# Optimization experiments

Hardware: AMD Instinct MI355X
Metric: run time of the kernel (lower is better)

## Reference

```python
import jax, jax.numpy as jnp
import numpy as np

# Static graph/model dims
G, NPG, N = 64, 200, 12800          # graphs, nodes/graph, total nodes
EPG, E = 1000, 64000                # edges/graph, total edges
D, H, C = 1024, 3, 1024             # feature_size, heads, out channels/head
K1, K2, K3 = 160, 80, 16            # topk sizes: ceil(.8*200), .5*160, .2*80
NEG = -1e9


def _gat(x, src, dst, mask, W, att_s, att_d, b):
    """PyG GATConv (concat heads, add_self_loops=True, leaky_relu 0.2)."""
    n = x.shape[0]
    xw = (x @ W).reshape(n, H, C)                 # [n,H,C]
    a_s = (xw * att_s).sum(-1)                    # [n,H]
    a_d = (xw * att_d).sum(-1)
    loop = jnp.arange(n, dtype=src.dtype)
    s = jnp.concatenate([src, loop])
    d = jnp.concatenate([dst, loop])
    m = jnp.concatenate([mask, jnp.ones((n,), bool)])
    logit = jax.nn.leaky_relu(a_s[s] + a_d[d], 0.2)   # [E+n,H]
    logit = jnp.where(m[:, None], logit, NEG)
    mx = jax.ops.segment_max(logit, d, num_segments=n)
    ex = jnp.where(m[:, None], jnp.exp(logit - mx[d]), 0.0)
    den = jax.ops.segment_sum(ex, d, num_segments=n)
    alpha = ex / (den[d] + 1e-16)                 # segment softmax over dst
    out = jax.ops.segment_sum(alpha[:, :, None] * xw[s], d, num_segments=n)
    return out.reshape(n, H * C) + b


def _topk(x, src, dst, mask, p, n_in, k):
    """PyG TopKPooling: score=tanh(x.p/||p||), keep top-k per graph,
    scale kept rows by score; edge filtering realized as a mask."""
    score = jnp.tanh((x @ p) / jnp.linalg.norm(p))
    vals, idx = jax.lax.top_k(score.reshape(G, n_in), k)     # [G,k]
    perm = (idx + jnp.arange(G)[:, None] * n_in).reshape(-1)
    new_x = x[perm] * vals.reshape(-1, 1)
    newid = jnp.full((G * n_in,), -1, jnp.int32).at[perm].set(
        jnp.arange(G * k, dtype=jnp.int32))
    ns, nd = newid[src], newid[dst]
    nm = mask & (ns >= 0) & (nd >= 0)
    return new_x, jnp.where(nm, ns, 0), jnp.where(nm, nd, 0), nm


def _readout(x, k):
    xg = x.reshape(G, k, C)                       # contiguous equal graphs
    return jnp.concatenate([xg.max(1), xg.mean(1)], axis=1)  # [G,2C]


def setup_inputs() -> dict:
    key = jax.random.key(0)
    ks = jax.random.split(key, 32)
    x = jax.random.normal(ks[0], (N, D), jnp.float32)
    gid = jnp.repeat(jnp.arange(G, dtype=jnp.int32), EPG)
    src = jax.random.randint(ks[1], (E,), 0, NPG, jnp.int32) + gid * NPG
    dst = jax.random.randint(ks[2], (E,), 0, NPG, jnp.int32) + gid * NPG
    edge_index = jnp.stack([src, dst])
    batch_index = jnp.repeat(jnp.arange(G, dtype=jnp.int32), NPG)
    edge_attr = jnp.zeros((E, 1), jnp.float32)

    def gl(k, shape, fan):
        return jax.random.normal(k, shape, jnp.float32) * (1.0 / np.sqrt(fan))

    inp = dict(x=x, edge_attr=edge_attr, edge_index=edge_index,
               batch_index=batch_index)
    i = 3
    for L, fin in ((1, D), (2, C), (3, C)):
        inp[f'W{L}'] = gl(ks[i], (fin, H * C), fin); i += 1
        inp[f'as{L}'] = gl(ks[i], (H, C), C); i += 1
        inp[f'ad{L}'] = gl(ks[i], (H, C), C); i += 1
        inp[f'b{L}'] = jnp.zeros((H * C,), jnp.float32)
        inp[f'Wt{L}'] = gl(ks[i], (H * C, C), H * C); i += 1
        inp[f'bt{L}'] = jnp.zeros((C,), jnp.float32)
        inp[f'p{L}'] = gl(ks[i], (C,), C); i += 1
    inp['Wl1'] = gl(ks[i], (2 * C, 1024), 2 * C); i += 1
    inp['bl1'] = jnp.zeros((1024,), jnp.float32)
    inp['Wl2'] = gl(ks[i], (1024, 2), 1024); i += 1
    inp['bl2'] = jnp.zeros((2,), jnp.float32)
    return inp


def reference(x, edge_attr, edge_index, batch_index,
              W1, as1, ad1, b1, Wt1, bt1, p1,
              W2, as2, ad2, b2, Wt2, bt2, p2,
              W3, as3, ad3, b3, Wt3, bt3, p3,
              Wl1, bl1, Wl2, bl2):
    src, dst = edge_index[0], edge_index[1]
    mask = jnp.ones((src.shape[0],), bool)
    h = _gat(x, src, dst, mask, W1, as1, ad1, b1) @ Wt1 + bt1
    h, src, dst, mask = _topk(h, src, dst, mask, p1, NPG, K1)
    r1 = _readout(h, K1)
    h = _gat(h, src, dst, mask, W2, as2, ad2, b2) @ Wt2 + bt2
    h, src, dst, mask = _topk(h, src, dst, mask, p2, K1, K2)
    r2 = _readout(h, K2)
    h = _gat(h, src, dst, mask, W3, as3, ad3, b3) @ Wt3 + bt3
    h, src, dst, mask = _topk(h, src, dst, mask, p3, K2, K3)
    r3 = _readout(h, K3)
    z = r1 + r2 + r3                               # [G, 2C]
    z = jax.nn.relu(z @ Wl1 + bl1)                 # dropout inactive (eval)
    return z @ Wl2 + bl2                           # [G, 2]
```

## Files before the change

### kernel.cpp

```cpp
#include <hip/hip_runtime.h>
#include <math.h>

#define NG 64
#define EE 64000
#define HC3 3072
#define CC 1024

static inline int cdiv(int a, int b) { return (a + b - 1) / b; }

typedef float f4_t __attribute__((ext_vector_type(4)));
typedef short s8_t __attribute__((ext_vector_type(8)));

__device__ __forceinline__ float lrelu(float x) { return x > 0.f ? x : 0.2f * x; }
__device__ __forceinline__ unsigned fenc(float f) {
    unsigned u = __float_as_uint(f);
    return (u & 0x80000000u) ? ~u : (u | 0x80000000u);
}
__device__ __forceinline__ float fdec(unsigned e) {
    return (e & 0x80000000u) ? __uint_as_float(e ^ 0x80000000u) : __uint_as_float(~e);
}
__device__ __forceinline__ unsigned short f2bf(float f) {
    unsigned u = __float_as_uint(f);
    u += 0x7fffu + ((u >> 16) & 1u);
    return (unsigned short)(u >> 16);
}
__device__ __forceinline__ float bf2f(unsigned short h) {
    return __uint_as_float(((unsigned)h) << 16);
}
__device__ __forceinline__ void gll16(const unsigned short* g, unsigned short* l) {
    __builtin_amdgcn_global_load_lds(
        (const __attribute__((address_space(1))) void*)g,
        (__attribute__((address_space(3))) void*)l, 16, 0, 0);
}

__global__ __launch_bounds__(256) void gemm_split(
    const unsigned short* __restrict__ Ahi, const unsigned short* __restrict__ Alo, int lda,
    const unsigned short* __restrict__ Bhi, const unsigned short* __restrict__ Blo, int ldb,
    float* __restrict__ C, int ldc, int K,
    size_t zsA, size_t zsB, size_t zsC)
{
    __shared__ unsigned short sAH[128 * 32];
    __shared__ unsigned short sAL[128 * 32];
    __shared__ unsigned short sBH[128 * 32];
    __shared__ unsigned short sBL[128 * 32];

    Ahi += blockIdx.z * zsA; Alo += blockIdx.z * zsA;
    Bhi += blockIdx.z * zsB; Blo += blockIdx.z * zsB;
    C   += blockIdx.z * zsC;

    const int t = threadIdx.x;
    const int w = t >> 6, lane = t & 63;
    const int wr = w >> 1, wc = w & 1;
    const int row0 = blockIdx.y * 128, col0 = blockIdx.x * 128;

    const int srow = w * 16 + (lane >> 2);
    const int skg = (((lane & 3) ^ ((lane >> 3) & 3)) << 3);
    const size_t aoff0 = (size_t)(row0 + srow) * lda + skg;
    const size_t aoff1 = (size_t)(row0 + 64 + srow) * lda + skg;
    const size_t boff0 = (size_t)(col0 + srow) * ldb + skg;
    const size_t boff1 = (size_t)(col0 + 64 + srow) * ldb + skg;
    const int l0 = (w * 16) * 32;
    const int l1 = (64 + w * 16) * 32;

    f4_t acc[4][4];
    const f4_t z4 = {0.f, 0.f, 0.f, 0.f};
#pragma unroll
    for (int i = 0; i < 4; ++i)
#pragma unroll
        for (int j = 0; j < 4; ++j) acc[i][j] = z4;

    const int mrow0 = wr * 64 + (lane & 15);
    const int nrow0 = wc * 64 + (lane & 15);
    const int kslot = (((lane >> 4) ^ ((lane >> 1) & 3)) << 3);

    for (int k0 = 0; k0 < K; k0 += 32) {
        gll16(Ahi + aoff0 + k0, &sAH[l0]);
        gll16(Ahi + aoff1 + k0, &sAH[l1]);
        gll16(Alo + aoff0 + k0, &sAL[l0]);
        gll16(Alo + aoff1 + k0, &sAL[l1]);
        gll16(Bhi + boff0 + k0, &sBH[l0]);
        gll16(Bhi + boff1 + k0, &sBH[l1]);
        gll16(Blo + boff0 + k0, &sBL[l0]);
        gll16(Blo + boff1 + k0, &sBL[l1]);
        __syncthreads();

        s8_t ah[4], al[4], bh[4], bl[4];
#pragma unroll
        for (int mt = 0; mt < 4; ++mt) {
            ah[mt] = *(const s8_t*)&sAH[(mrow0 + mt * 16) * 32 + kslot];
            al[mt] = *(const s8_t*)&sAL[(mrow0 + mt * 16) * 32 + kslot];
        }
#pragma unroll
        for (int nt = 0; nt < 4; ++nt) {
            bh[nt] = *(const s8_t*)&sBH[(nrow0 + nt * 16) * 32 + kslot];
            bl[nt] = *(const s8_t*)&sBL[(nrow0 + nt * 16) * 32 + kslot];
        }
#pragma unroll
        for (int mt = 0; mt < 4; ++mt)
#pragma unroll
            for (int nt = 0; nt < 4; ++nt) {
                acc[mt][nt] = __builtin_amdgcn_mfma_f32_16x16x32_bf16(ah[mt], bh[nt], acc[mt][nt], 0, 0, 0);
                acc[mt][nt] = __builtin_amdgcn_mfma_f32_16x16x32_bf16(ah[mt], bl[nt], acc[mt][nt], 0, 0, 0);
                acc[mt][nt] = __builtin_amdgcn_mfma_f32_16x16x32_bf16(al[mt], bh[nt], acc[mt][nt], 0, 0, 0);
            }
        __syncthreads();
    }

#pragma unroll
    for (int mt = 0; mt < 4; ++mt) {
        int row = row0 + wr * 64 + mt * 16 + (lane >> 4) * 4;
#pragma unroll
        for (int nt = 0; nt < 4; ++nt) {
            int col = col0 + wc * 64 + nt * 16 + (lane & 15);
#pragma unroll
            for (int r = 0; r < 4; ++r)
                C[(size_t)(row + r) * ldc + col] = acc[mt][nt][r];
        }
    }
}

__global__ __launch_bounds__(256) void gemm_splitk(
    const unsigned short* __restrict__ Ahi, const unsigned short* __restrict__ Alo, int lda,
    const unsigned short* __restrict__ Bhi, const unsigned short* __restrict__ Blo, int ldb,
    float* __restrict__ C, int ldc, int ksub)
{
    __shared__ unsigned short sAH[128 * 32];
    __shared__ unsigned short sAL[128 * 32];
    __shared__ unsigned short sBH[128 * 32];
    __shared__ unsigned short sBL[128 * 32];

    const int t = threadIdx.x;
    const int w = t >> 6, lane = t & 63;
    const int wr = w >> 1, wc = w & 1;
    const int row0 = blockIdx.x * 128, col0 = blockIdx.y * 128;
    const int kbase = blockIdx.z * ksub;

    const int srow = w * 16 + (lane >> 2);
    const int skg = (((lane & 3) ^ ((lane >> 3) & 3)) << 3);
    const size_t aoff0 = (size_t)(row0 + srow) * lda + skg;
    const size_t aoff1 = (size_t)(row0 + 64 + srow) * lda + skg;
    const size_t boff0 = (size_t)(col0 + srow) * ldb + skg;
    const size_t boff1 = (size_t)(col0 + 64 + srow) * ldb + skg;
    const int l0 = (w * 16) * 32;
    const int l1 = (64 + w * 16) * 32;

    f4_t acc[4][4];
    const f4_t z4 = {0.f, 0.f, 0.f, 0.f};
#pragma unroll
    for (int i = 0; i < 4; ++i)
#pragma unroll
        for (int j = 0; j < 4; ++j) acc[i][j] = z4;

    const int mrow0 = wr * 64 + (lane & 15);
    const int nrow0 = wc * 64 + (lane & 15);
    const int kslot = (((lane >> 4) ^ ((lane >> 1) & 3)) << 3);

    for (int k0 = kbase; k0 < kbase + ksub; k0 += 32) {
        gll16(Ahi + aoff0 + k0, &sAH[l0]);
        gll16(Ahi + aoff1 + k0, &sAH[l1]);
        gll16(Alo + aoff0 + k0, &sAL[l0]);
        gll16(Alo + aoff1 + k0, &sAL[l1]);
        gll16(Bhi + boff0 + k0, &sBH[l0]);
        gll16(Bhi + boff1 + k0, &sBH[l1]);
        gll16(Blo + boff0 + k0, &sBL[l0]);
        gll16(Blo + boff1 + k0, &sBL[l1]);
        __syncthreads();

        s8_t ah[4], al[4], bh[4], bl[4];
#pragma unroll
        for (int mt = 0; mt < 4; ++mt) {
            ah[mt] = *(const s8_t*)&sAH[(mrow0 + mt * 16) * 32 + kslot];
            al[mt] = *(const s8_t*)&sAL[(mrow0 + mt * 16) * 32 + kslot];
        }
#pragma unroll
        for (int nt = 0; nt < 4; ++nt) {
            bh[nt] = *(const s8_t*)&sBH[(nrow0 + nt * 16) * 32 + kslot];
            bl[nt] = *(const s8_t*)&sBL[(nrow0 + nt * 16) * 32 + kslot];
        }
#pragma unroll
        for (int mt = 0; mt < 4; ++mt)
#pragma unroll
            for (int nt = 0; nt < 4; ++nt) {
                acc[mt][nt] = __builtin_amdgcn_mfma_f32_16x16x32_bf16(ah[mt], bh[nt], acc[mt][nt], 0, 0, 0);
                acc[mt][nt] = __builtin_amdgcn_mfma_f32_16x16x32_bf16(ah[mt], bl[nt], acc[mt][nt], 0, 0, 0);
                acc[mt][nt] = __builtin_amdgcn_mfma_f32_16x16x32_bf16(al[mt], bh[nt], acc[mt][nt], 0, 0, 0);
            }
        __syncthreads();
    }

#pragma unroll
    for (int mt = 0; mt < 4; ++mt) {
        int row = row0 + wr * 64 + mt * 16 + (lane >> 4) * 4;
#pragma unroll
        for (int nt = 0; nt < 4; ++nt) {
            int col = col0 + wc * 64 + nt * 16 + (lane & 15);
#pragma unroll
            for (int r = 0; r < 4; ++r)
                atomicAdd(&C[(size_t)(row + r) * ldc + col], acc[mt][nt][r]);
        }
    }
}

__global__ __launch_bounds__(256) void finalize_xn(float* __restrict__ XN,
    const float* __restrict__ BV, const float* __restrict__ vals)
{
    int r = blockIdx.x, t = threadIdx.x;
    float v = vals[r];
    float4* p = (float4*)(XN + (size_t)r * CC);
    const float4* b = (const float4*)BV;
    float4 x = p[t], bb = b[t];
    x.x = (x.x + bb.x) * v; x.y = (x.y + bb.y) * v;
    x.z = (x.z + bb.z) * v; x.w = (x.w + bb.w) * v;
    p[t] = x;
}

__global__ void split_w_all(const float* __restrict__ w0, const float* __restrict__ w1,
    const float* __restrict__ w2, int lbase,
    unsigned short* __restrict__ ohi, unsigned short* __restrict__ olo)
{
    const float* Wp[3] = {w0, w1, w2};
    int slot = blockIdx.y;
    int L = lbase + slot / 3, h = slot % 3;
    int idx = blockIdx.x * 256 + threadIdx.x;
    int r = idx >> 10, c = idx & 1023;
    float v = Wp[L][(size_t)r * HC3 + h * CC + c];
    unsigned short hh = f2bf(v);
    ohi[(size_t)slot * 1048576 + idx] = hh;
    olo[(size_t)slot * 1048576 + idx] = f2bf(v - bf2f(hh));
}

__global__ void transpose_split_wt_all(const float* __restrict__ w0,
    const float* __restrict__ w1, const float* __restrict__ w2, int lbase,
    unsigned short* __restrict__ ohi, unsigned short* __restrict__ olo)
{
    const float* Wp[3] = {w0, w1, w2};
    int slot = blockIdx.z;
    int L = lbase + slot / 3, h = slot % 3;
    __shared__ float tile[32][33];
    int t = threadIdx.x, tr = t >> 5, tc = t & 31;
    int r0 = blockIdx.y * 32, c0 = blockIdx.x * 32;
    const float* in = Wp[L] + (size_t)h * 1048576;
#pragma unroll
    for (int i = 0; i < 4; ++i)
        tile[tr + i * 8][tc] = in[(size_t)(r0 + tr + i * 8) * CC + c0 + tc];
    __syncthreads();
    unsigned short* oh = ohi + (size_t)slot * 1048576;
    unsigned short* ol = olo + (size_t)slot * 1048576;
#pragma unroll
    for (int i = 0; i < 4; ++i) {
        int oc = c0 + tr + i * 8;
        int orr = r0 + tc;
        float v = tile[tc][tr + i * 8];
        unsigned short hh = f2bf(v);
        oh[(size_t)oc * CC + orr] = hh;
        ol[(size_t)oc * CC + orr] = f2bf(v - bf2f(hh));
    }
}

__global__ void split_interleave_all(const float* __restrict__ in,
    unsigned short* __restrict__ ohi, unsigned short* __restrict__ olo)
{
    int slot = blockIdx.y;
    int lrel = slot / 3, h = slot % 3;
    int idx = blockIdx.x * 256 + threadIdx.x;
    int c = idx >> 10, d = idx & 1023;
    float v = in[(size_t)slot * 1048576 + idx];
    unsigned short hh = f2bf(v);
    size_t dst = (size_t)lrel * 3145728 + (size_t)c * HC3 + h * CC + d;
    ohi[dst] = hh;
    olo[dst] = f2bf(v - bf2f(hh));
}

__global__ void qzero(float* __restrict__ q, int n) {
    int i = blockIdx.x * 256 + threadIdx.x;
    if (i < n) q[i] = 0.f;
}

__global__ void qvec_all(const float* __restrict__ MHT, const float* __restrict__ p0,
    const float* __restrict__ p1, const float* __restrict__ p2, int lbase,
    float* __restrict__ q)
{
    const float* Pp[3] = {p0, p1, p2};
    int slot = blockIdx.z;
    int L = lbase + slot / 3, h = slot % 3;
    int d = blockIdx.x * 256 + threadIdx.x;
    int c0 = blockIdx.y * 128;
    const float* m = MHT + (size_t)slot * 1048576 + (size_t)c0 * CC + d;
    const float* p = Pp[L];
    float s = 0.f;
#pragma unroll 8
    for (int c = 0; c < 128; ++c) s += m[(size_t)c * CC] * p[c0 + c];
    atomicAdd(&q[(size_t)L * HC3 + h * CC + d], s);
}

__global__ __launch_bounds__(256) void attvec_all(const float* __restrict__ w0,
    const float* __restrict__ w1, const float* __restrict__ w2,
    const float* __restrict__ as0, const float* __restrict__ as1, const float* __restrict__ as2,
    const float* __restrict__ ad0, const float* __restrict__ ad1, const float* __restrict__ ad2,
    int lbase, float* __restrict__ asv, float* __restrict__ adv)
{
    const float* Wp[3] = {w0, w1, w2};
    const float* Sp[3] = {as0, as1, as2};
    const float* Dp[3] = {ad0, ad1, ad2};
    int L = lbase + blockIdx.y;
    int wid = blockIdx.x * 4 + (threadIdx.x >> 6);
    int lane = threadIdx.x & 63;
    int h = wid >> 10, kk = wid & 1023;
    const float* wr = Wp[L] + (long long)kk * HC3 + h * CC;
    const float* sa = Sp[L] + h * CC;
    const float* da = Dp[L] + h * CC;
    float ss = 0.f, dd = 0.f;
    for (int c = lane; c < CC; c += 64) { float w = wr[c]; ss += w * sa[c]; dd += w * da[c]; }
    for (int off = 32; off; off >>= 1) { ss += __shfl_xor(ss, off, 64); dd += __shfl_xor(dd, off, 64); }
    if (lane == 0) { asv[(size_t)L * HC3 + h * CC + kk] = ss; adv[(size_t)L * HC3 + h * CC + kk] = dd; }
}

__global__ __launch_bounds__(256) void attn_node(const float* __restrict__ xin,
    const float* __restrict__ asv, const float* __restrict__ adv, const float* __restrict__ q,
    float* __restrict__ AS, float* __restrict__ AD, float* __restrict__ T3,
    float* __restrict__ sl, unsigned* __restrict__ mxe, float* __restrict__ sexp,
    int* __restrict__ cnt, int* __restrict__ cur, int n)
{
    int node = blockIdx.x * 4 + (threadIdx.x >> 6);
    int lane = threadIdx.x & 63;
    if (node >= n) return;
    const float* xr = xin + (long long)node * CC;
    float s0 = 0, s1 = 0, s2 = 0, d0 = 0, d1 = 0, d2 = 0, t0 = 0, t1 = 0, t2 = 0;
    for (int j = lane; j < CC; j += 64) {
        float v = xr[j];
        s0 += v * asv[j]; s1 += v * asv[CC + j]; s2 += v * asv[2 * CC + j];
        d0 += v * adv[j]; d1 += v * adv[CC + j]; d2 += v * adv[2 * CC + j];
        t0 += v * q[j];   t1 += v * q[CC + j];   t2 += v * q[2 * CC + j];
    }
    for (int off = 32; off; off >>= 1) {
        s0 += __shfl_xor(s0, off, 64); s1 += __shfl_xor(s1, off, 64); s2 += __shfl_xor(s2, off, 64);
        d0 += __shfl_xor(d0, off, 64); d1 += __shfl_xor(d1, off, 64); d2 += __shfl_xor(d2, off, 64);
        t0 += __shfl_xor(t0, off, 64); t1 += __shfl_xor(t1, off, 64); t2 += __shfl_xor(t2, off, 64);
    }
    if (lane == 0) {
        AS[node * 3 + 0] = s0; AS[node * 3 + 1] = s1; AS[node * 3 + 2] = s2;
        AD[node * 3 + 0] = d0; AD[node * 3 + 1] = d1; AD[node * 3 + 2] = d2;
        T3[node * 3 + 0] = t0; T3[node * 3 + 1] = t1; T3[node * 3 + 2] = t2;
        float l0v = lrelu(s0 + d0), l1v = lrelu(s1 + d1), l2v = lrelu(s2 + d2);
        sl[node * 3 + 0] = l0v; sl[node * 3 + 1] = l1v; sl[node * 3 + 2] = l2v;
        mxe[node * 3 + 0] = fenc(l0v); mxe[node * 3 + 1] = fenc(l1v); mxe[node * 3 + 2] = fenc(l2v);
        sexp[node * 3 + 0] = 0.f; sexp[node * 3 + 1] = 0.f; sexp[node * 3 + 2] = 0.f;
        cnt[node] = 0; cur[node] = 0;
    }
}

__global__ void bvinit_pnorm(const float* __restrict__ bt0, const float* __restrict__ bt1,
    const float* __restrict__ bt2, const float* __restrict__ p0, const float* __restrict__ p1,
    const float* __restrict__ p2, int lbase, float* __restrict__ BV, float* __restrict__ PN)
{
    const float* Bp[3] = {bt0, bt1, bt2};
    const float* Pp[3] = {p0, p1, p2};
    int L = lbase + blockIdx.y;
    if (blockIdx.x < 4) {
        int c = blockIdx.x * 256 + threadIdx.x;
        BV[(size_t)L * CC + c] = Bp[L][c];
    } else {
        __shared__ float red[256];
        int t = threadIdx.x;
        const float* p = Pp[L];
        float s = 0.f;
        for (int j = t; j < CC; j += 256) { float v = p[j]; s += v * v; }
        red[t] = s; __syncthreads();
        for (int off = 128; off; off >>= 1) { if (t < off) red[t] += red[t + off]; __syncthreads(); }
        if (t == 0) PN[L] = sqrtf(red[0]);
    }
}

__global__ void bvec_part(const float* __restrict__ b0, const float* __restrict__ b1,
    const float* __restrict__ b2, const float* __restrict__ wt0, const float* __restrict__ wt1,
    const float* __restrict__ wt2, int lbase, float* __restrict__ BV)
{
    const float* bp[3] = {b0, b1, b2};
    const float* wp[3] = {wt0, wt1, wt2};
    int L = lbase + blockIdx.z;
    int c = blockIdx.x * 256 + threadIdx.x;
    int k0 = blockIdx.y * 256;
    const float* b = bp[L];
    const float* Wt = wp[L];
    float acc = 0.f;
#pragma unroll 8
    for (int k = k0; k < k0 + 256; ++k) acc += b[k] * Wt[(size_t)k * CC + c];
    atomicAdd(&BV[(size_t)L * CC + c], acc);
}

__global__ void bvp_all(const float* __restrict__ BV, const float* __restrict__ p0,
    const float* __restrict__ p1, const float* __restrict__ p2, int lbase,
    float* __restrict__ BVP)
{
    const float* Pp[3] = {p0, p1, p2};
    int L = lbase + blockIdx.x;
    __shared__ float red[256];
    int t = threadIdx.x;
    const float* p = Pp[L];
    float s = 0.f;
    for (int j = t; j < CC; j += 256) s += BV[(size_t)L * CC + j] * p[j];
    red[t] = s; __syncthreads();
    for (int off = 128; off; off >>= 1) { if (t < off) red[t] += red[t + off]; __syncthreads(); }
    if (t == 0) BVP[L] = red[0];
}

__global__ void edge_pass1(const int* __restrict__ src, const int* __restrict__ dst,
    const int* __restrict__ msk, const float* __restrict__ AS, const float* __restrict__ AD,
    unsigned* __restrict__ mxe, float* __restrict__ sexp, int* __restrict__ cnt)
{
    int e = blockIdx.x * 256 + threadIdx.x;
    if (e >= EE || !msk[e]) return;
    int s = src[e], d = dst[e];
    atomicAdd(&cnt[d], 1);
#pragma unroll
    for (int h = 0; h < 3; ++h) {
        float l = lrelu(AS[s * 3 + h] + AD[d * 3 + h]);
        atomicMax(&mxe[d * 3 + h], fenc(l));
        atomicAdd(&sexp[d * 3 + h], expf(l));
    }
}

__global__ void scan_graph(const int* __restrict__ cnt, int* __restrict__ offs,
    int* __restrict__ gt, int npg)
{
    if (threadIdx.x != 0) return;
    int g = blockIdx.x, base = g * npg, run = 0;
    for (int i = 0; i < npg; ++i) { offs[base + i] = run; run += cnt[base + i]; }
    gt[g] = run;
}

__global__ void scan_finish(int* __restrict__ offs, const int* __restrict__ gt, int n, int npg)
{
    int i = blockIdx.x * 256 + threadIdx.x;
    if (i >= n) return;
    int g = i / npg;
    int base = 0;
    for (int gg = 0; gg < g; ++gg) base += gt[gg];
    offs[i] += base;
}

__global__ void decode_selfden(const unsigned* __restrict__ mxe, const float* __restrict__ sl,
    const float* __restrict__ sexp, float* __restrict__ mxf, float* __restrict__ den, int n)
{
    int i = blockIdx.x * 256 + threadIdx.x;
    if (i >= n) return;
#pragma unroll
    for (int h = 0; h < 3; ++h) {
        float m = fdec(mxe[i * 3 + h]);
        mxf[i * 3 + h] = m;
        den[i * 3 + h] = expf(sl[i * 3 + h] - m) + expf(-m) * sexp[i * 3 + h];
    }
}

__global__ void fill_alpha(const int* __restrict__ src, const int* __restrict__ dst,
    const int* __restrict__ msk, const int* __restrict__ offs, int* __restrict__ cur,
    const float* __restrict__ AS, const float* __restrict__ AD,
    const float* __restrict__ mxf, const float* __restrict__ den,
    int* __restrict__ csrs, float* __restrict__ csra)
{
    int e = blockIdx.x * 256 + threadIdx.x;
    if (e >= EE || !msk[e]) return;
    int s = src[e], d = dst[e];
    int pos = offs[d] + atomicAdd(&cur[d], 1);
    csrs[pos] = s;
#pragma unroll
    for (int h = 0; h < 3; ++h) {
        float l = lrelu(AS[s * 3 + h] + AD[d * 3 + h]);
        float ex = expf(l - mxf[d * 3 + h]);
        csra[pos * 3 + h] = ex / (den[d * 3 + h] + 1e-16f);
    }
}

__global__ __launch_bounds__(64) void score_topk(const float* __restrict__ T3,
    const float* __restrict__ sl, const float* __restrict__ mxf, const float* __restrict__ den,
    const int* __restrict__ offs, const int* __restrict__ cnt, const int* __restrict__ csrs,
    const float* __restrict__ csra, const float* __restrict__ bvp, const float* __restrict__ pn,
    int npg, int k, int* __restrict__ perm, float* __restrict__ vals, int* __restrict__ newid)
{
    __shared__ float sc[256];
    int g = blockIdx.x, lane = threadIdx.x;
    float bv0 = bvp[0], pn0 = pn[0];
    for (int ii = lane; ii < npg; ii += 64) {
        int i = g * npg + ii;
        float s = 0.f;
#pragma unroll
        for (int h = 0; h < 3; ++h) {
            float aself = expf(sl[i * 3 + h] - mxf[i * 3 + h]) / (den[i * 3 + h] + 1e-16f);
            s += aself * T3[i * 3 + h];
        }
        int beg = offs[i], num = cnt[i];
        for (int e = 0; e < num; ++e) {
            int sn = csrs[beg + e];
#pragma unroll
            for (int h = 0; h < 3; ++h) s += csra[(beg + e) * 3 + h] * T3[sn * 3 + h];
        }
        sc[ii] = tanhf((s + bv0) / pn0);
        newid[i] = -1;
    }
    __syncthreads();
    float v[4];
    int nsl = (npg + 63) >> 6;
#pragma unroll
    for (int s2 = 0; s2 < 4; ++s2) {
        int idx = lane + (s2 << 6);
        v[s2] = (s2 < nsl && idx < npg) ? sc[idx] : -1e30f;
    }
    for (int j = 0; j < k; ++j) {
        float bv = -2e30f; int bi = 0x7fffffff;
#pragma unroll
        for (int s2 = 0; s2 < 4; ++s2) {
            int idx = lane + (s2 << 6);
            if (v[s2] > bv) { bv = v[s2]; bi = idx; }
        }
        for (int off = 32; off; off >>= 1) {
            float ov = __shfl_xor(bv, off, 64);
            int   oi = __shfl_xor(bi, off, 64);
            if (ov > bv || (ov == bv && oi < bi)) { bv = ov; bi = oi; }
        }
        if (lane == 0) {
            perm[g * k + j] = g * npg + bi;
            vals[g * k + j] = bv;
            newid[g * npg + bi] = g * k + j;
        }
        if ((bi & 63) == lane) v[bi >> 6] = -1e30f;
    }
}

__global__ __launch_bounds__(256) void aggregate_sel(const float* __restrict__ xin,
    const float* __restrict__ sl, const float* __restrict__ mxf, const float* __restrict__ den,
    const int* __restrict__ offs, const int* __restrict__ cnt,
    const int* __restrict__ csrs, const float* __restrict__ csra,
    const int* __restrict__ perm,
    unsigned short* __restrict__ ahi, unsigned short* __restrict__ alo)
{
    int r = blockIdx.x, t = threadIdx.x;
    int i = perm[r];
    float aself[3];
#pragma unroll
    for (int h = 0; h < 3; ++h)
        aself[h] = expf(sl[i * 3 + h] - mxf[i * 3 + h]) / (den[i * 3 + h] + 1e-16f);
    const float* xr = xin + (long long)i * CC;
    float acc[3][4];
#pragma unroll
    for (int j = 0; j < 4; ++j) {
        float v = xr[t + (j << 8)];
#pragma unroll
        for (int h = 0; h < 3; ++h) acc[h][j] = aself[h] * v;
    }
    int beg = offs[i], num = cnt[i];
    for (int e = 0; e < num; ++e) {
        int s = csrs[beg + e];
        float a0 = csra[(beg + e) * 3 + 0];
        float a1 = csra[(beg + e) * 3 + 1];
        float a2 = csra[(beg + e) * 3 + 2];
        const float* sr = xin + (long long)s * CC;
#pragma unroll
        for (int j = 0; j < 4; ++j) {
            float v = sr[t + (j << 8)];
            acc[0][j] += a0 * v; acc[1][j] += a1 * v; acc[2][j] += a2 * v;
        }
    }
#pragma unroll
    for (int h = 0; h < 3; ++h)
#pragma unroll
        for (int j = 0; j < 4; ++j) {
            int c = t + (j << 8);
            float v = acc[h][j];
            unsigned short hh = f2bf(v);
            size_t idx = (size_t)r * HC3 + h * CC + c;
            ahi[idx] = hh;
            alo[idx] = f2bf(v - bf2f(hh));
        }
}

__global__ void remap_edges(int* __restrict__ s, int* __restrict__ d,
    int* __restrict__ m, const int* __restrict__ newid)
{
    int e = blockIdx.x * 256 + threadIdx.x;
    if (e >= EE) return;
    if (!m[e]) { s[e] = 0; d[e] = 0; return; }
    int ns = newid[s[e]], nd = newid[d[e]];
    int nm = (ns >= 0 && nd >= 0) ? 1 : 0;
    m[e] = nm; s[e] = nm ? ns : 0; d[e] = nm ? nd : 0;
}

__global__ __launch_bounds__(256) void readout_part(const float* __restrict__ xn,
    int k, float* __restrict__ PM, float* __restrict__ PS)
{
    int g = blockIdx.x, ch = blockIdx.y, t = threadIdx.x;
    int rpc = k >> 3, r0 = ch * rpc;
#pragma unroll
    for (int j = 0; j < 4; ++j) {
        int c = t + (j << 8);
        float mx = -1e30f, sm = 0.f;
        for (int r = r0; r < r0 + rpc; ++r) {
            float vv = xn[((size_t)(g * k + r)) * CC + c];
            mx = fmaxf(mx, vv); sm += vv;
        }
        PM[(size_t)(g * 8 + ch) * CC + c] = mx;
        PS[(size_t)(g * 8 + ch) * CC + c] = sm;
    }
}

__global__ __launch_bounds__(256) void readout_fin(const float* __restrict__ PM,
    const float* __restrict__ PS, int k, float* __restrict__ R)
{
    int g = blockIdx.x, t = threadIdx.x;
#pragma unroll
    for (int j = 0; j < 4; ++j) {
        int c = t + (j << 8);
        float mx = -1e30f, sm = 0.f;
#pragma unroll
        for (int ch = 0; ch < 8; ++ch) {
            mx = fmaxf(mx, PM[(size_t)(g * 8 + ch) * CC + c]);
            sm += PS[(size_t)(g * 8 + ch) * CC + c];
        }
        R[g * 2048 + c] = mx;
        R[g * 2048 + 1024 + c] = sm / (float)k;
    }
}

__global__ void copy_edges(const int* __restrict__ ei, int* __restrict__ s,
    int* __restrict__ d, int* __restrict__ m)
{
    int e = blockIdx.x * 256 + threadIdx.x;
    if (e >= EE) return;
    s[e] = ei[e]; d[e] = ei[EE + e]; m[e] = 1;
}

__global__ void zsum(const float* __restrict__ a, const float* __restrict__ b,
    const float* __restrict__ c, float* __restrict__ z)
{
    int i = blockIdx.x * 256 + threadIdx.x;
    if (i < NG * 2048) z[i] = a[i] + b[i] + c[i];
}

__global__ __launch_bounds__(256) void mlp1_kernel(const float* __restrict__ Z,
    const float* __restrict__ Wl1, const float* __restrict__ bl1, float* __restrict__ Z1)
{
    int c = blockIdx.x * 256 + threadIdx.x;
    int g = blockIdx.y;
    float acc = bl1[c];
    const float* zr = Z + g * 2048;
    for (int kk = 0; kk < 2048; ++kk) acc += zr[kk] * Wl1[kk * 1024 + c];
    Z1[g * 1024 + c] = acc > 0.f ? acc : 0.f;
}

__global__ __launch_bounds__(64) void mlp2_kernel(const float* __restrict__ Z1,
    const float* __restrict__ Wl2, const float* __restrict__ bl2, float* __restrict__ out)
{
    int b = blockIdx.x; int g = b >> 1, o = b & 1;
    int lane = threadIdx.x;
    const float* zr = Z1 + g * 1024;
    float s = 0.f;
    for (int j = lane; j < 1024; j += 64) s += zr[j] * Wl2[j * 2 + o];
    for (int off = 32; off; off >>= 1) s += __shfl_xor(s, off, 64);
    if (lane == 0) out[g * 2 + o] = s + bl2[o];
}

extern "C" void kernel_launch(void* const* d_in, const int* in_sizes, int n_in,
                              void* d_out, int out_size, void* d_ws, size_t ws_size,
                              hipStream_t stream)
{
    const float* x   = (const float*)d_in[0];
    const int*   ei  = (const int*)d_in[2];
    const float* W[3]    = {(const float*)d_in[4],  (const float*)d_in[11], (const float*)d_in[18]};
    const float* atts[3] = {(const float*)d_in[5],  (const float*)d_in[12], (const float*)d_in[19]};
    const float* attd[3] = {(const float*)d_in[6],  (const float*)d_in[13], (const float*)d_in[20]};
    const float* bb[3]   = {(const float*)d_in[7],  (const float*)d_in[14], (const float*)d_in[21]};
    const float* Wt[3]   = {(const float*)d_in[8],  (const float*)d_in[15], (const float*)d_in[22]};
    const float* bt[3]   = {(const float*)d_in[9],  (const float*)d_in[16], (const float*)d_in[23]};
    const float* pv[3]   = {(const float*)d_in[10], (const float*)d_in[17], (const float*)d_in[24]};
    const float* Wl1 = (const float*)d_in[25];
    const float* bl1 = (const float*)d_in[26];
    const float* Wl2 = (const float*)d_in[27];
    const float* bl2 = (const float*)d_in[28];
    float* out = (float*)d_out;

    const bool batched = ws_size >= (size_t)225 * 1024 * 1024;

    char* wp = (char*)d_ws;
    auto carve = [&](size_t bytes) -> void* {
        void* p = (void*)wp;
        wp += (bytes + 255) & ~(size_t)255;
        return p;
    };
    const int NMAX = 12800;
    const int GKMAX = 10240;
    const size_t MSZ = (size_t)CC * CC;
    const int NSLOT = batched ? 9 : 3;
    unsigned short* A2H = (unsigned short*)carve((size_t)GKMAX * HC3 * 2);
    unsigned short* A2L = (unsigned short*)carve((size_t)GKMAX * HC3 * 2);
    unsigned short* WTH = (unsigned short*)A2H;
    unsigned short* WTL = WTH + (size_t)NSLOT * MSZ;
    unsigned short* WSH = WTL + (size_t)NSLOT * MSZ;
    unsigned short* WSL = (unsigned short*)A2L;
    float* MHT = (float*)(WSL + (size_t)NSLOT * MSZ);
    float* XN   = (float*)carve((size_t)GKMAX * CC * 4);
    unsigned short* B2H = (unsigned short*)carve((size_t)NSLOT * MSZ * 2);
    unsigned short* B2L = (unsigned short*)carve((size_t)NSLOT * MSZ * 2);
    float* PM   = (float*)carve((size_t)NG * 8 * CC * 4);
    float* PS   = (float*)carve((size_t)NG * 8 * CC * 4);
    float* ASV  = (float*)carve((size_t)3 * HC3 * 4);
    float* ADV  = (float*)carve((size_t)3 * HC3 * 4);
    float* QV   = (float*)carve((size_t)3 * HC3 * 4);
    float* BV   = (float*)carve((size_t)3 * CC * 4);
    float* AS   = (float*)carve((size_t)NMAX * 3 * 4);
    float* AD   = (float*)carve((size_t)NMAX * 3 * 4);
    float* T3   = (float*)carve((size_t)NMAX * 3 * 4);
    float* SL   = (float*)carve((size_t)NMAX * 3 * 4);
    unsigned* MXE = (unsigned*)carve((size_t)NMAX * 3 * 4);
    float* MXF  = (float*)carve((size_t)NMAX * 3 * 4);
    float* DEN  = (float*)carve((size_t)NMAX * 3 * 4);
    float* SEXP = (float*)carve((size_t)NMAX * 3 * 4);
    int* CNT    = (int*)carve((size_t)NMAX * 4);
    int* OFFS   = (int*)carve((size_t)NMAX * 4);
    int* CUR    = (int*)carve((size_t)NMAX * 4);
    int* NEWID  = (int*)carve((size_t)NMAX * 4);
    int* GT     = (int*)carve((size_t)NG * 4);
    int* CSRS   = (int*)carve((size_t)EE * 4);
    float* CSRA = (float*)carve((size_t)EE * 3 * 4);
    int* SRC = (int*)carve((size_t)EE * 4);
    int* DST = (int*)carve((size_t)EE * 4);
    int* MK  = (int*)carve((size_t)EE * 4);
    int* PERM  = (int*)carve((size_t)GKMAX * 4);
    float* VALS = (float*)carve((size_t)GKMAX * 4);
    float* PN  = (float*)carve(256);
    float* BVP = (float*)carve(256);
    float* R0 = (float*)carve((size_t)NG * 2048 * 4);
    float* R1 = (float*)carve((size_t)NG * 2048 * 4);
    float* R2 = (float*)carve((size_t)NG * 2048 * 4);
    float* Z  = (float*)carve((size_t)NG * 2048 * 4);
    float* Z1 = (float*)carve((size_t)NG * 1024 * 4);
    float* Rarr[3] = {R0, R1, R2};
    (void)in_sizes; (void)n_in; (void)out_size;

    copy_edges<<<cdiv(EE, 256), 256, 0, stream>>>(ei, SRC, DST, MK);

    auto prep = [&](int lbase, int nl) {
        int nslots = 3 * nl;
        split_w_all<<<dim3(4096, nslots), 256, 0, stream>>>(W[0], W[1], W[2], lbase, WSH, WSL);
        transpose_split_wt_all<<<dim3(32, 32, nslots), 256, 0, stream>>>(Wt[0], Wt[1], Wt[2],
                                                                          lbase, WTH, WTL);
        gemm_split<<<dim3(8, 8, nslots), 256, 0, stream>>>(WTH, WTL, CC, WSH, WSL, CC,
            MHT, CC, CC, MSZ, MSZ, MSZ);
        split_interleave_all<<<dim3(4096, nslots), 256, 0, stream>>>(MHT, B2H, B2L);
        qzero<<<cdiv(nl * HC3, 256), 256, 0, stream>>>(QV + (size_t)lbase * HC3, nl * HC3);
        qvec_all<<<dim3(4, 8, nslots), 256, 0, stream>>>(MHT, pv[0], pv[1], pv[2], lbase, QV);
        attvec_all<<<dim3(768, nl), 256, 0, stream>>>(W[0], W[1], W[2],
            atts[0], atts[1], atts[2], attd[0], attd[1], attd[2], lbase, ASV, ADV);
        bvinit_pnorm<<<dim3(5, nl), 256, 0, stream>>>(bt[0], bt[1], bt[2],
            pv[0], pv[1], pv[2], lbase, BV, PN);
        bvec_part<<<dim3(4, 12, nl), 256, 0, stream>>>(bb[0], bb[1], bb[2],
            Wt[0], Wt[1], Wt[2], lbase, BV);
        bvp_all<<<nl, 256, 0, stream>>>(BV, pv[0], pv[1], pv[2], lbase, BVP);
    };

    if (batched) prep(0, 3);

    const int ns_[3]  = {12800, 10240, 5120};
    const int npg_[3] = {200, 160, 80};
    const int kk_[3]  = {160, 80, 16};
    const int sk_[3]  = {2, 2, 4};
    const float* xin = x;

    for (int L = 0; L < 3; ++L) {
        int n = ns_[L], npg = npg_[L], k = kk_[L];
        int gk = NG * k;
        if (!batched) prep(L, 1);
        size_t b2off = batched ? (size_t)L * 3 * MSZ : 0;
        attn_node<<<n / 4, 256, 0, stream>>>(xin, ASV + (size_t)L * HC3,
            ADV + (size_t)L * HC3, QV + (size_t)L * HC3, AS, AD, T3,
            SL, MXE, SEXP, CNT, CUR, n);
        edge_pass1<<<cdiv(EE, 256), 256, 0, stream>>>(SRC, DST, MK, AS, AD, MXE, SEXP, CNT);
        scan_graph<<<NG, 64, 0, stream>>>(CNT, OFFS, GT, npg);
        scan_finish<<<cdiv(n, 256), 256, 0, stream>>>(OFFS, GT, n, npg);
        decode_selfden<<<cdiv(n, 256), 256, 0, stream>>>(MXE, SL, SEXP, MXF, DEN, n);
        fill_alpha<<<cdiv(EE, 256), 256, 0, stream>>>(SRC, DST, MK, OFFS, CUR,
                                                      AS, AD, MXF, DEN, CSRS, CSRA);
        score_topk<<<NG, 64, 0, stream>>>(T3, SL, MXF, DEN, OFFS, CNT, CSRS, CSRA,
                                          BVP + L, PN + L, npg, k, PERM, VALS, NEWID);
        aggregate_sel<<<gk, 256, 0, stream>>>(xin, SL, MXF, DEN, OFFS, CNT, CSRS, CSRA,
                                              PERM, A2H, A2L);
        hipMemsetAsync(XN, 0, (size_t)gk * CC * 4, stream);
        gemm_splitk<<<dim3(gk / 128, 8, sk_[L]), 256, 0, stream>>>(A2H, A2L, HC3,
            B2H + b2off, B2L + b2off, HC3, XN, CC, HC3 / sk_[L]);
        finalize_xn<<<gk, 256, 0, stream>>>(XN, BV + (size_t)L * CC, VALS);
        readout_part<<<dim3(NG, 8), 256, 0, stream>>>(XN, k, PM, PS);
        readout_fin<<<NG, 256, 0, stream>>>(PM, PS, k, Rarr[L]);
        if (L < 2) remap_edges<<<cdiv(EE, 256), 256, 0, stream>>>(SRC, DST, MK, NEWID);
        xin = XN;
    }

    zsum<<<cdiv(NG * 2048, 256), 256, 0, stream>>>(R0, R1, R2, Z);
    mlp1_kernel<<<dim3(4, NG), 256, 0, stream>>>(Z, Wl1, bl1, Z1);
    mlp2_kernel<<<NG * 2, 64, 0, stream>>>(Z1, Wl2, bl2, out);
}
```

Before: 1.386 ms.

## Fuse weight-prep, scan, finalize and readout kernels; reassociate q-vector computation

The prep GEMM now writes bf16 hi/lo split interleaved output directly, which removes the fp32 intermediate and the separate split_interleave pass. The q vector is reassociated as W·(Wt·p) via a new wtp_all kernel, with the dot product folded into attvec, so the qzero, qvec and atomic passes go away. The per-graph scan becomes a wave-parallel shuffle scan merged with decode; bias/score scaling moves into readout_part; zsum is folded into mlp1. Together these cut launches and memory passes, with small changes in floating-point summation order.

```diff
diff --git a/kernel.cpp b/kernel.cpp
--- a/kernel.cpp
+++ b/kernel.cpp
@@ -33,20 +33,21 @@
         (__attribute__((address_space(3))) void*)l, 16, 0, 0);
 }
 
-__global__ __launch_bounds__(256) void gemm_split(
-    const unsigned short* __restrict__ Ahi, const unsigned short* __restrict__ Alo, int lda,
-    const unsigned short* __restrict__ Bhi, const unsigned short* __restrict__ Blo, int ldb,
-    float* __restrict__ C, int ldc, int K,
-    size_t zsA, size_t zsB, size_t zsC)
+__global__ __launch_bounds__(256) void gemm_prep(
+    const unsigned short* __restrict__ Ahi, const unsigned short* __restrict__ Alo,
+    const unsigned short* __restrict__ Bhi, const unsigned short* __restrict__ Blo,
+    unsigned short* __restrict__ ohi, unsigned short* __restrict__ olo, int K)
 {
     __shared__ unsigned short sAH[128 * 32];
     __shared__ unsigned short sAL[128 * 32];
     __shared__ unsigned short sBH[128 * 32];
     __shared__ unsigned short sBL[128 * 32];
 
-    Ahi += blockIdx.z * zsA; Alo += blockIdx.z * zsA;
-    Bhi += blockIdx.z * zsB; Blo += blockIdx.z * zsB;
-    C   += blockIdx.z * zsC;
+    const size_t MSZ = (size_t)CC * CC;
+    const int slot = blockIdx.z;
+    const int lrel = slot / 3, hh = slot % 3;
+    Ahi += slot * MSZ; Alo += slot * MSZ;
+    Bhi += slot * MSZ; Blo += slot * MSZ;
 
     const int t = threadIdx.x;
     const int w = t >> 6, lane = t & 63;
@@ -55,10 +56,10 @@
 
     const int srow = w * 16 + (lane >> 2);
     const int skg = (((lane & 3) ^ ((lane >> 3) & 3)) << 3);
-    const size_t aoff0 = (size_t)(row0 + srow) * lda + skg;
-    const size_t aoff1 = (size_t)(row0 + 64 + srow) * lda + skg;
-    const size_t boff0 = (size_t)(col0 + srow) * ldb + skg;
-    const size_t boff1 = (size_t)(col0 + 64 + srow) * ldb + skg;
+    const size_t aoff0 = (size_t)(row0 + srow) * CC + skg;
+    const size_t aoff1 = (size_t)(row0 + 64 + srow) * CC + skg;
+    const size_t boff0 = (size_t)(col0 + srow) * CC + skg;
+    const size_t boff1 = (size_t)(col0 + 64 + srow) * CC + skg;
     const int l0 = (w * 16) * 32;
     const int l1 = (64 + w * 16) * 32;
 
@@ -113,8 +114,13 @@
         for (int nt = 0; nt < 4; ++nt) {
             int col = col0 + wc * 64 + nt * 16 + (lane & 15);
 #pragma unroll
-            for (int r = 0; r < 4; ++r)
-                C[(size_t)(row + r) * ldc + col] = acc[mt][nt][r];
+            for (int r = 0; r < 4; ++r) {
+                float v = acc[mt][nt][r];
+                unsigned short hv = f2bf(v);
+                size_t dst = (size_t)lrel * 3 * MSZ + (size_t)(row + r) * HC3 + hh * CC + col;
+                ohi[dst] = hv;
+                olo[dst] = f2bf(v - bf2f(hv));
+            }
         }
     }
 }
@@ -201,19 +207,6 @@
     }
 }
 
-__global__ __launch_bounds__(256) void finalize_xn(float* __restrict__ XN,
-    const float* __restrict__ BV, const float* __restrict__ vals)
-{
-    int r = blockIdx.x, t = threadIdx.x;
-    float v = vals[r];
-    float4* p = (float4*)(XN + (size_t)r * CC);
-    const float4* b = (const float4*)BV;
-    float4 x = p[t], bb = b[t];
-    x.x = (x.x + bb.x) * v; x.y = (x.y + bb.y) * v;
-    x.z = (x.z + bb.z) * v; x.w = (x.w + bb.w) * v;
-    p[t] = x;
-}
-
 __global__ void split_w_all(const float* __restrict__ w0, const float* __restrict__ w1,
     const float* __restrict__ w2, int lbase,
     unsigned short* __restrict__ ohi, unsigned short* __restrict__ olo)
@@ -257,47 +250,30 @@
     }
 }
 
-__global__ void split_interleave_all(const float* __restrict__ in,
-    unsigned short* __restrict__ ohi, unsigned short* __restrict__ olo)
-{
-    int slot = blockIdx.y;
-    int lrel = slot / 3, h = slot % 3;
-    int idx = blockIdx.x * 256 + threadIdx.x;
-    int c = idx >> 10, d = idx & 1023;
-    float v = in[(size_t)slot * 1048576 + idx];
-    unsigned short hh = f2bf(v);
-    size_t dst = (size_t)lrel * 3145728 + (size_t)c * HC3 + h * CC + d;
-    ohi[dst] = hh;
-    olo[dst] = f2bf(v - bf2f(hh));
-}
-
-__global__ void qzero(float* __restrict__ q, int n) {
-    int i = blockIdx.x * 256 + threadIdx.x;
-    if (i < n) q[i] = 0.f;
-}
-
-__global__ void qvec_all(const float* __restrict__ MHT, const float* __restrict__ p0,
-    const float* __restrict__ p1, const float* __restrict__ p2, int lbase,
-    float* __restrict__ q)
-{
+__global__ __launch_bounds__(256) void wtp_all(const float* __restrict__ wt0,
+    const float* __restrict__ wt1, const float* __restrict__ wt2,
+    const float* __restrict__ p0, const float* __restrict__ p1, const float* __restrict__ p2,
+    int lbase, float* __restrict__ U)
+{
+    const float* Wp[3] = {wt0, wt1, wt2};
     const float* Pp[3] = {p0, p1, p2};
-    int slot = blockIdx.z;
-    int L = lbase + slot / 3, h = slot % 3;
-    int d = blockIdx.x * 256 + threadIdx.x;
-    int c0 = blockIdx.y * 128;
-    const float* m = MHT + (size_t)slot * 1048576 + (size_t)c0 * CC + d;
+    int wid = blockIdx.x * 4 + (threadIdx.x >> 6);
+    int lane = threadIdx.x & 63;
+    int L = lbase + wid / HC3, rr = wid % HC3;
+    const float* row = Wp[L] + (size_t)rr * CC;
     const float* p = Pp[L];
     float s = 0.f;
-#pragma unroll 8
-    for (int c = 0; c < 128; ++c) s += m[(size_t)c * CC] * p[c0 + c];
-    atomicAdd(&q[(size_t)L * HC3 + h * CC + d], s);
+    for (int c = lane; c < CC; c += 64) s += row[c] * p[c];
+    for (int off = 32; off; off >>= 1) s += __shfl_xor(s, off, 64);
+    if (lane == 0) U[(size_t)L * HC3 + rr] = s;
 }
 
 __global__ __launch_bounds__(256) void attvec_all(const float* __restrict__ w0,
     const float* __restrict__ w1, const float* __restrict__ w2,
     const float* __restrict__ as0, const float* __restrict__ as1, const float* __restrict__ as2,
     const float* __restrict__ ad0, const float* __restrict__ ad1, const float* __restrict__ ad2,
-    int lbase, float* __restrict__ asv, float* __restrict__ adv)
+    const float* __restrict__ U, int lbase,
+    float* __restrict__ asv, float* __restrict__ adv, float* __restrict__ qv)
 {
     const float* Wp[3] = {w0, w1, w2};
     const float* Sp[3] = {as0, as1, as2};
@@ -309,10 +285,20 @@
     const float* wr = Wp[L] + (long long)kk * HC3 + h * CC;
     const float* sa = Sp[L] + h * CC;
     const float* da = Dp[L] + h * CC;
-    float ss = 0.f, dd = 0.f;
-    for (int c = lane; c < CC; c += 64) { float w = wr[c]; ss += w * sa[c]; dd += w * da[c]; }
-    for (int off = 32; off; off >>= 1) { ss += __shfl_xor(ss, off, 64); dd += __shfl_xor(dd, off, 64); }
-    if (lane == 0) { asv[(size_t)L * HC3 + h * CC + kk] = ss; adv[(size_t)L * HC3 + h * CC + kk] = dd; }
+    const float* ua = U + (size_t)L * HC3 + h * CC;
+    float ss = 0.f, dd = 0.f, qq = 0.f;
+    for (int c = lane; c < CC; c += 64) {
+        float w = wr[c];
+        ss += w * sa[c]; dd += w * da[c]; qq += w * ua[c];
+    }
+    for (int off = 32; off; off >>= 1) {
+        ss += __shfl_xor(ss, off, 64); dd += __shfl_xor(dd, off, 64); qq += __shfl_xor(qq, off, 64);
+    }
+    if (lane == 0) {
+        asv[(size_t)L * HC3 + h * CC + kk] = ss;
+        adv[(size_t)L * HC3 + h * CC + kk] = dd;
+        qv[(size_t)L * HC3 + h * CC + kk] = qq;
+    }
 }
 
 __global__ __launch_bounds__(256) void attn_node(const float* __restrict__ xin,
@@ -420,16 +406,30 @@
     }
 }
 
-__global__ void scan_graph(const int* __restrict__ cnt, int* __restrict__ offs,
-    int* __restrict__ gt, int npg)
-{
-    if (threadIdx.x != 0) return;
-    int g = blockIdx.x, base = g * npg, run = 0;
-    for (int i = 0; i < npg; ++i) { offs[base + i] = run; run += cnt[base + i]; }
-    gt[g] = run;
-}
-
-__global__ void scan_finish(int* __restrict__ offs, const int* __restrict__ gt, int n, int npg)
+__global__ __launch_bounds__(64) void scan_graph(const int* __restrict__ cnt,
+    int* __restrict__ offs, int* __restrict__ gt, int npg)
+{
+    int g = blockIdx.x, lane = threadIdx.x;
+    int run = 0;
+    for (int c0 = 0; c0 < npg; c0 += 64) {
+        int i = c0 + lane;
+        int v = (i < npg) ? cnt[g * npg + i] : 0;
+        int s = v;
+#pragma unroll
+        for (int off = 1; off < 64; off <<= 1) {
+            int o = __shfl_up(s, off, 64);
+            if (lane >= off) s += o;
+        }
+        if (i < npg) offs[g * npg + i] = run + s - v;
+        run += __shfl(s, 63, 64);
+    }
+    if (lane == 0) gt[g] = run;
+}
+
+__global__ void post_edge(int* __restrict__ offs, const int* __restrict__ gt,
+    const unsigned* __restrict__ mxe, const float* __restrict__ sl,
+    const float* __restrict__ sexp, float* __restrict__ mxf, float* __restrict__ den,
+    int n, int npg)
 {
     int i = blockIdx.x * 256 + threadIdx.x;
     if (i >= n) return;
@@ -437,13 +437,6 @@
     int base = 0;
     for (int gg = 0; gg < g; ++gg) base += gt[gg];
     offs[i] += base;
-}
-
-__global__ void decode_selfden(const unsigned* __restrict__ mxe, const float* __restrict__ sl,
-    const float* __restrict__ sexp, float* __restrict__ mxf, float* __restrict__ den, int n)
-{
-    int i = blockIdx.x * 256 + threadIdx.x;
-    if (i >= n) return;
 #pragma unroll
     for (int h = 0; h < 3; ++h) {
         float m = fdec(mxe[i * 3 + h]);
@@ -584,32 +577,36 @@
     m[e] = nm; s[e] = nm ? ns : 0; d[e] = nm ? nd : 0;
 }
 
-__global__ __launch_bounds__(256) void readout_part(const float* __restrict__ xn,
+__global__ __launch_bounds__(256) void readout_part(float* __restrict__ xn,
+    const float* __restrict__ BV, const float* __restrict__ vals,
     int k, float* __restrict__ PM, float* __restrict__ PS)
 {
     int g = blockIdx.x, ch = blockIdx.y, t = threadIdx.x;
     int rpc = k >> 3, r0 = ch * rpc;
+#pragma unroll
+    for (int j = 0; j < 4; ++j) {
+        int c = t + (j << 8);
+        float bvc = BV[c];
+        float mx = -1e30f, sm = 0.f;
+        for (int r = r0; r < r0 + rpc; ++r) {
+            size_t idx = ((size_t)(g * k + r)) * CC + c;
+            float vv = (xn[idx] + bvc) * vals[g * k + r];
+            xn[idx] = vv;
+            mx = fmaxf(mx, vv); sm += vv;
+        }
+        PM[(size_t)(g * 8 + ch) * CC + c] = mx;
+        PS[(size_t)(g * 8 + ch) * CC + c] = sm;
+    }
+}
+
+__global__ __launch_bounds__(256) void readout_fin(const float* __restrict__ PM,
+    const float* __restrict__ PS, int k, float* __restrict__ R)
+{
+    int g = blockIdx.x, t = threadIdx.x;
 #pragma unroll
     for (int j = 0; j < 4; ++j) {
         int c = t + (j << 8);
         float mx = -1e30f, sm = 0.f;
-        for (int r = r0; r < r0 + rpc; ++r) {
-            float vv = xn[((size_t)(g * k + r)) * CC + c];
-            mx = fmaxf(mx, vv); sm += vv;
-        }
-        PM[(size_t)(g * 8 + ch) * CC + c] = mx;
-        PS[(size_t)(g * 8 + ch) * CC + c] = sm;
-    }
-}
-
-__global__ __launch_bounds__(256) void readout_fin(const float* __restrict__ PM,
-    const float* __restrict__ PS, int k, float* __restrict__ R)
-{
-    int g = blockIdx.x, t = threadIdx.x;
-#pragma unroll
-    for (int j = 0; j < 4; ++j) {
-        int c = t + (j << 8);
-        float mx = -1e30f, sm = 0.f;
 #pragma unroll
         for (int ch = 0; ch < 8; ++ch) {
             mx = fmaxf(mx, PM[(size_t)(g * 8 + ch) * CC + c]);
@@ -628,21 +625,18 @@
     s[e] = ei[e]; d[e] = ei[EE + e]; m[e] = 1;
 }
 
-__global__ void zsum(const float* __restrict__ a, const float* __restrict__ b,
-    const float* __restrict__ c, float* __restrict__ z)
-{
-    int i = blockIdx.x * 256 + threadIdx.x;
-    if (i < NG * 2048) z[i] = a[i] + b[i] + c[i];
-}
-
-__global__ __launch_bounds__(256) void mlp1_kernel(const float* __restrict__ Z,
+__global__ __launch_bounds__(256) void mlp1_kernel(const float* __restrict__ R0,
+    const float* __restrict__ R1, const float* __restrict__ R2,
     const float* __restrict__ Wl1, const float* __restrict__ bl1, float* __restrict__ Z1)
 {
     int c = blockIdx.x * 256 + threadIdx.x;
     int g = blockIdx.y;
     float acc = bl1[c];
-    const float* zr = Z + g * 2048;
-    for (int kk = 0; kk < 2048; ++kk) acc += zr[kk] * Wl1[kk * 1024 + c];
+    const float* r0 = R0 + g * 2048;
+    const float* r1 = R1 + g * 2048;
+    const float* r2 = R2 + g * 2048;
+    for (int kk = 0; kk < 2048; ++kk)
+        acc += (r0[kk] + r1[kk] + r2[kk]) * Wl1[kk * 1024 + c];
     Z1[g * 1024 + c] = acc > 0.f ? acc : 0.f;
 }
 
@@ -695,7 +689,6 @@
     unsigned short* WTL = WTH + (size_t)NSLOT * MSZ;
     unsigned short* WSH = WTL + (size_t)NSLOT * MSZ;
     unsigned short* WSL = (unsigned short*)A2L;
-    float* MHT = (float*)(WSL + (size_t)NSLOT * MSZ);
     float* XN   = (float*)carve((size_t)GKMAX * CC * 4);
     unsigned short* B2H = (unsigned short*)carve((size_t)NSLOT * MSZ * 2);
     unsigned short* B2L = (unsigned short*)carve((size_t)NSLOT * MSZ * 2);
@@ -704,6 +697,7 @@
     float* ASV  = (float*)carve((size_t)3 * HC3 * 4);
     float* ADV  = (float*)carve((size_t)3 * HC3 * 4);
     float* QV   = (float*)carve((size_t)3 * HC3 * 4);
+    float* UU   = (float*)carve((size_t)3 * HC3 * 4);
     float* BV   = (float*)carve((size_t)3 * CC * 4);
     float* AS   = (float*)carve((size_t)NMAX * 3 * 4);
     float* AD   = (float*)carve((size_t)NMAX * 3 * 4);
@@ -730,7 +724,6 @@
     float* R0 = (float*)carve((size_t)NG * 2048 * 4);
     float* R1 = (float*)carve((size_t)NG * 2048 * 4);
     float* R2 = (float*)carve((size_t)NG * 2048 * 4);
-    float* Z  = (float*)carve((size_t)NG * 2048 * 4);
     float* Z1 = (float*)carve((size_t)NG * 1024 * 4);
     float* Rarr[3] = {R0, R1, R2};
     (void)in_sizes; (void)n_in; (void)out_size;
@@ -742,13 +735,11 @@
         split_w_all<<<dim3(4096, nslots), 256, 0, stream>>>(W[0], W[1], W[2], lbase, WSH, WSL);
         transpose_split_wt_all<<<dim3(32, 32, nslots), 256, 0, stream>>>(Wt[0], Wt[1], Wt[2],
                                                                           lbase, WTH, WTL);
-        gemm_split<<<dim3(8, 8, nslots), 256, 0, stream>>>(WTH, WTL, CC, WSH, WSL, CC,
-            MHT, CC, CC, MSZ, MSZ, MSZ);
-        split_interleave_all<<<dim3(4096, nslots), 256, 0, stream>>>(MHT, B2H, B2L);
-        qzero<<<cdiv(nl * HC3, 256), 256, 0, stream>>>(QV + (size_t)lbase * HC3, nl * HC3);
-        qvec_all<<<dim3(4, 8, nslots), 256, 0, stream>>>(MHT, pv[0], pv[1], pv[2], lbase, QV);
+        wtp_all<<<nl * 768, 256, 0, stream>>>(Wt[0], Wt[1], Wt[2], pv[0], pv[1], pv[2],
+                                              lbase, UU);
+        gemm_prep<<<dim3(8, 8, nslots), 256, 0, stream>>>(WTH, WTL, WSH, WSL, B2H, B2L, CC);
         attvec_all<<<dim3(768, nl), 256, 0, stream>>>(W[0], W[1], W[2],
-            atts[0], atts[1], atts[2], attd[0], attd[1], attd[2], lbase, ASV, ADV);
+            atts[0], atts[1], atts[2], attd[0], attd[1], attd[2], UU, lbase, ASV, ADV, QV);
         bvinit_pnorm<<<dim3(5, nl), 256, 0, stream>>>(bt[0], bt[1], bt[2],
             pv[0], pv[1], pv[2], lbase, BV, PN);
         bvec_part<<<dim3(4, 12, nl), 256, 0, stream>>>(bb[0], bb[1], bb[2],
@@ -774,8 +765,7 @@
             SL, MXE, SEXP, CNT, CUR, n);
         edge_pass1<<<cdiv(EE, 256), 256, 0, stream>>>(SRC, DST, MK, AS, AD, MXE, SEXP, CNT);
         scan_graph<<<NG, 64, 0, stream>>>(CNT, OFFS, GT, npg);
-        scan_finish<<<cdiv(n, 256), 256, 0, stream>>>(OFFS, GT, n, npg);
-        decode_selfden<<<cdiv(n, 256), 256, 0, stream>>>(MXE, SL, SEXP, MXF, DEN, n);
+        post_edge<<<cdiv(n, 256), 256, 0, stream>>>(OFFS, GT, MXE, SL, SEXP, MXF, DEN, n, npg);
         fill_alpha<<<cdiv(EE, 256), 256, 0, stream>>>(SRC, DST, MK, OFFS, CUR,
                                                       AS, AD, MXF, DEN, CSRS, CSRA);
         score_topk<<<NG, 64, 0, stream>>>(T3, SL, MXF, DEN, OFFS, CNT, CSRS, CSRA,
@@ -785,14 +775,13 @@
         hipMemsetAsync(XN, 0, (size_t)gk * CC * 4, stream);
         gemm_splitk<<<dim3(gk / 128, 8, sk_[L]), 256, 0, stream>>>(A2H, A2L, HC3,
             B2H + b2off, B2L + b2off, HC3, XN, CC, HC3 / sk_[L]);
-        finalize_xn<<<gk, 256, 0, stream>>>(XN, BV + (size_t)L * CC, VALS);
-        readout_part<<<dim3(NG, 8), 256, 0, stream>>>(XN, k, PM, PS);
+        readout_part<<<dim3(NG, 8), 256, 0, stream>>>(XN, BV + (size_t)L * CC, VALS,
+                                                      k, PM, PS);
         readout_fin<<<NG, 256, 0, stream>>>(PM, PS, k, Rarr[L]);
         if (L < 2) remap_edges<<<cdiv(EE, 256), 256, 0, stream>>>(SRC, DST, MK, NEWID);
         xin = XN;
     }
 
-    zsum<<<cdiv(NG * 2048, 256), 256, 0, stream>>>(R0, R1, R2, Z);
-    mlp1_kernel<<<dim3(4, NG), 256, 0, stream>>>(Z, Wl1, bl1, Z1);
+    mlp1_kernel<<<dim3(4, NG), 256, 0, stream>>>(R0, R1, R2, Wl1, bl1, Z1);
     mlp2_kernel<<<NG * 2, 64, 0, stream>>>(Z1, Wl2, bl2, out);
 }
```

Result: faster. 1.335 ms (-3.7%).
